# Kernel optimization log

Measured on AMD Instinct MI355X. Metric: run time of the kernel, lower is better.

Reference implementation:

```python
import jax, jax.numpy as jnp
import numpy as np

B, H, S, D = 2, 16, 2048, 64

def setup_inputs() -> dict:
    key = jax.random.key(0)
    kq, kk, kv = jax.random.split(key, 3)
    Q = jax.random.normal(kq, (B, H, S, D), dtype=jnp.float32)
    K = jax.random.normal(kk, (B, H, S, D), dtype=jnp.float32)
    V = jax.random.normal(kv, (B, H, S, D), dtype=jnp.float32)
    # causal mask, broadcastable over batch/head dims (True = keep)
    mask = jnp.tril(jnp.ones((S, S), dtype=jnp.bool_))
    return {"Q": Q, "K": K, "V": V, "mask": mask}

def reference(Q, K, V, mask):
    scale = jax.lax.rsqrt(jnp.float32(Q.shape[-1]))
    # [b, h, q, k] attention logits
    at = jnp.einsum('bhqd,bhkd->bhqk', Q, K) * scale
    at = jnp.where(mask, at, -jnp.inf)
    # manual numerically-stable softmax (matches SoftMax module)
    x_max = jnp.max(at, axis=-1, keepdims=True)
    x_exp = jnp.exp(at - x_max)
    scores = x_exp / jnp.sum(x_exp, axis=-1, keepdims=True)
    return jnp.einsum('bhqk,bhkd->bhqd', scores, V)
```

## Files before the change

### kernel.cpp

```cpp
#include <hip/hip_runtime.h>
#include <math.h>

typedef __attribute__((ext_vector_type(8))) short bf16x8;
typedef __attribute__((ext_vector_type(8))) short s16x8;
typedef __attribute__((ext_vector_type(4))) short s16x4;
typedef __attribute__((ext_vector_type(4))) float f32x4;
typedef __attribute__((ext_vector_type(16))) float f32x16;

namespace {
constexpr int kS   = 2048;
constexpr int kD   = 64;
constexpr int kBH  = 32;
constexpr int kT   = kS / 64;
constexpr int PPAD = 72;
constexpr float kScaleLog2e = 0.125f * 1.44269504088896340736f;
}

__device__ __forceinline__ short f2bf(float f) {
    union { float f; unsigned u; } c; c.f = f;
    unsigned r = c.u + 0x7fffu + ((c.u >> 16) & 1u);
    return (short)(r >> 16);
}

__device__ __forceinline__ s16x8 pack8(const float4& a, const float4& b) {
    s16x8 r;
    r[0] = f2bf(a.x); r[1] = f2bf(a.y); r[2] = f2bf(a.z); r[3] = f2bf(a.w);
    r[4] = f2bf(b.x); r[5] = f2bf(b.y); r[6] = f2bf(b.z); r[7] = f2bf(b.w);
    return r;
}

__device__ __forceinline__ unsigned cvtpk(float lo, float hi_) {
    unsigned r;
    asm("v_cvt_pk_bf16_f32 %0, %1, %2" : "=v"(r) : "v"(lo), "v"(hi_));
    return r;
}
__device__ __forceinline__ void plswap(unsigned& a, unsigned& b) {
    asm("v_permlane32_swap_b32 %0, %1" : "+v"(a), "+v"(b));
}

__global__ __launch_bounds__(256)
void prepack(const float* __restrict__ K, const float* __restrict__ V,
             short* __restrict__ wsK, short* __restrict__ wsVT)
{
    __shared__ float vt[64][65];
    const int tid = threadIdx.x;
    const int kb  = blockIdx.x;
    const int bh  = blockIdx.y;
    const int r   = tid >> 2;
    const int s   = tid & 3;
    const int c0  = s * 16;

    const size_t grow = ((size_t)bh * kS + (size_t)kb * 64 + r) * kD + c0;
    const size_t tbase = ((size_t)bh * kT + kb) * 4096;

    {
        const float4* kr = (const float4*)(K + grow);
        float4 a = kr[0], b = kr[1], c = kr[2], d = kr[3];
        const int kt = r >> 5, ql = r & 31;
        short* out = wsK + tbase + (size_t)((s * 2 + kt) * 64) * 8;
        *(s16x8*)(out + (size_t)ql * 8)        = pack8(a, b);
        *(s16x8*)(out + (size_t)(32 + ql) * 8) = pack8(c, d);
    }
    {
        const float4* vr = (const float4*)(V + grow);
        float4 a = vr[0], b = vr[1], c = vr[2], d = vr[3];
        float t[16] = {a.x,a.y,a.z,a.w, b.x,b.y,b.z,b.w,
                       c.x,c.y,c.z,c.w, d.x,d.y,d.z,d.w};
        #pragma unroll
        for (int jj = 0; jj < 16; ++jj) vt[r][c0 + jj] = t[jj];
    }
    __syncthreads();
    {
        const int d     = tid >> 2;
        const int slice = tid & 3;
        const int k0    = slice * 16;
        const int dt = d >> 5, ql = d & 31;
        s16x8 g0, g1;
        #pragma unroll
        for (int jj = 0; jj < 8; ++jj) g0[jj] = f2bf(vt[k0 + jj][d]);
        #pragma unroll
        for (int jj = 0; jj < 8; ++jj) g1[jj] = f2bf(vt[k0 + 8 + jj][d]);
        short* out = wsVT + tbase + (size_t)((slice * 2 + dt) * 64) * 8;
        *(s16x8*)(out + (size_t)ql * 8)        = g0;
        *(s16x8*)(out + (size_t)(32 + ql) * 8) = g1;
    }
}

__global__ __launch_bounds__(64)
void attn_pair(const float* __restrict__ Q, const short* __restrict__ wsK,
               const short* __restrict__ wsVT, float* __restrict__ O)
{
    const int lane = threadIdx.x & 63;
    const int ql   = lane & 31;
    const int hi   = lane >> 5;

    const int n    = (int)blockIdx.x;
    const int xcd  = n & 7;
    const int rest = n >> 3;
    const int bh   = xcd * 4 + (rest >> 5);
    const int p    = rest & 31;

    const char* Kroot = (const char*)wsK + (size_t)bh * kT * 8192;
    const char* Vroot = (const char*)wsVT + (size_t)bh * kT * 8192;

    f32x16 zero16;
    #pragma unroll
    for (int c = 0; c < 16; ++c) zero16[c] = 0.f;

    auto loadK = [&](int kb, bf16x8 (&kf)[8]) {
        const char* kp = Kroot + (size_t)kb * 8192 + lane * 16;
        #pragma unroll
        for (int i = 0; i < 8; ++i)
            kf[i] = *(const bf16x8*)(kp + i * 1024);
    };

    #pragma unroll 1
    for (int sidx = 0; sidx < 2; ++sidx) {
        const int qs   = sidx == 0 ? 63 - p : p;
        const int T    = (qs >> 1) + 1;
        const int qrow = qs * 32 + ql;

        const float* Qr = Q + ((size_t)bh * kS + qrow) * kD;
        bf16x8 qf[4];
        #pragma unroll
        for (int s = 0; s < 4; ++s) {
            const float4 a = *(const float4*)(Qr + s * 16 + hi * 8);
            const float4 b = *(const float4*)(Qr + s * 16 + hi * 8 + 4);
            bf16x8 f;
            f[0] = f2bf(a.x * kScaleLog2e); f[1] = f2bf(a.y * kScaleLog2e);
            f[2] = f2bf(a.z * kScaleLog2e); f[3] = f2bf(a.w * kScaleLog2e);
            f[4] = f2bf(b.x * kScaleLog2e); f[5] = f2bf(b.y * kScaleLog2e);
            f[6] = f2bf(b.z * kScaleLog2e); f[7] = f2bf(b.w * kScaleLog2e);
            qf[s] = f;
        }

        f32x16 o[2] = {zero16, zero16};
        float l_ = 0.f;

        bf16x8 kA[8], kB[8];
        loadK(0, kA);

        auto tile = [&](bf16x8 (&kcur)[8], bf16x8 (&knxt)[8], int kb) {
            bf16x8 vf[8];
            {
                const char* vp = Vroot + (size_t)kb * 8192 + lane * 16;
                #pragma unroll
                for (int i = 0; i < 8; ++i)
                    vf[i] = *(const bf16x8*)(vp + i * 1024);
            }

            f32x16 sacc[2] = {zero16, zero16};
            #pragma unroll
            for (int kt = 0; kt < 2; ++kt)
                #pragma unroll
                for (int s = 0; s < 4; ++s)
                    sacc[kt] = __builtin_amdgcn_mfma_f32_32x32x16_bf16(
                        kcur[s * 2 + kt], qf[s], sacc[kt], 0, 0, 0);

            if (kb + 1 < T) loadK(kb + 1, knxt);

            if (kb == T - 1) {
                #pragma unroll
                for (int kt = 0; kt < 2; ++kt) {
                    const int kbase = kb * 64 + kt * 32 + 4 * hi;
                    #pragma unroll
                    for (int c = 0; c < 16; ++c) {
                        const int kg = kbase + (c & 3) + 8 * (c >> 2);
                        if (kg > qrow) sacc[kt][c] = -1e30f;
                    }
                }
            }

            float psum = 0.f;
            #pragma unroll
            for (int kt = 0; kt < 2; ++kt)
                #pragma unroll
                for (int c = 0; c < 16; ++c) {
                    const float pe = exp2f(sacc[kt][c]);
                    sacc[kt][c] = pe;
                    psum += pe;
                }
            l_ += psum;

            #pragma unroll
            for (int kt = 0; kt < 2; ++kt) {
                unsigned w8[8];
                #pragma unroll
                for (int i = 0; i < 8; ++i)
                    w8[i] = cvtpk(sacc[kt][2 * i], sacc[kt][2 * i + 1]);
                #pragma unroll
                for (int s = 0; s < 2; ++s) {
                    unsigned A0 = w8[4 * s + 0], B0 = w8[4 * s + 2];
                    unsigned A1 = w8[4 * s + 1], B1 = w8[4 * s + 3];
                    plswap(A0, B0);
                    plswap(A1, B1);
                    union { unsigned u[4]; bf16x8 v; } pk;
                    pk.u[0] = A0; pk.u[1] = A1; pk.u[2] = B0; pk.u[3] = B1;
                    #pragma unroll
                    for (int dt = 0; dt < 2; ++dt)
                        o[dt] = __builtin_amdgcn_mfma_f32_32x32x16_bf16(
                            vf[(kt * 2 + s) * 2 + dt], pk.v, o[dt], 0, 0, 0);
                }
            }
        };

        int kb = 0;
        #pragma unroll 1
        while (true) {
            tile(kA, kB, kb);
            if (++kb == T) break;
            tile(kB, kA, kb);
            if (++kb == T) break;
        }

        const float l   = l_ + __shfl_xor(l_, 32);
        const float inv = 1.0f / l;
        float* Ob = O + ((size_t)bh * kS + qrow) * kD;
        #pragma unroll
        for (int dt = 0; dt < 2; ++dt)
            #pragma unroll
            for (int t = 0; t < 4; ++t) {
                float4 v;
                v.x = o[dt][4 * t + 0] * inv;
                v.y = o[dt][4 * t + 1] * inv;
                v.z = o[dt][4 * t + 2] * inv;
                v.w = o[dt][4 * t + 3] * inv;
                *(float4*)(Ob + dt * 32 + 4 * hi + 8 * t) = v;
            }
    }
}

__global__ __launch_bounds__(256)
void attn_mfma(const float* __restrict__ Q, const float* __restrict__ K,
               const float* __restrict__ V, float* __restrict__ O)
{
    __shared__ short Klds[64 * PPAD];
    __shared__ short VTlds[64 * PPAD];
    __shared__ short Plds[4 * 16 * PPAD];

    const int tid  = threadIdx.x;
    const int lane = tid & 63;
    const int w    = tid >> 6;
    const int lo   = lane & 15;
    const int hi   = lane >> 4;
    const int qt = (int)gridDim.x - 1 - (int)blockIdx.x;
    const int bh = blockIdx.y;
    const size_t hbase = (size_t)bh * kS * kD;

    const float* Qr = Q + hbase + (size_t)(qt * 64 + w * 16 + lo) * kD;
    bf16x8 qfrag[2];
    #pragma unroll
    for (int dc = 0; dc < 2; ++dc) {
        const float4 a = *(const float4*)(Qr + dc * 32 + hi * 8);
        const float4 b = *(const float4*)(Qr + dc * 32 + hi * 8 + 4);
        bf16x8 f;
        f[0] = f2bf(a.x * kScaleLog2e); f[1] = f2bf(a.y * kScaleLog2e);
        f[2] = f2bf(a.z * kScaleLog2e); f[3] = f2bf(a.w * kScaleLog2e);
        f[4] = f2bf(b.x * kScaleLog2e); f[5] = f2bf(b.y * kScaleLog2e);
        f[6] = f2bf(b.z * kScaleLog2e); f[7] = f2bf(b.w * kScaleLog2e);
        qfrag[dc] = f;
    }

    const f32x4 zero4 = {0.f, 0.f, 0.f, 0.f};
    f32x4 o[4] = {zero4, zero4, zero4, zero4};
    float m_[4] = {-1e30f, -1e30f, -1e30f, -1e30f};
    float l_[4] = {0.f, 0.f, 0.f, 0.f};
    const int sr = tid >> 2;
    const int sc = (tid & 3) * 16;
    const float* Kg = K + hbase;
    const float* Vg = V + hbase;
    short* Pw = &Plds[w * 16 * PPAD];

    for (int kb = 0; kb <= qt; ++kb) {
        __syncthreads();
        {
            const float* krow = Kg + (size_t)(kb * 64 + sr) * kD + sc;
            const float* vrow = Vg + (size_t)(kb * 64 + sr) * kD + sc;
            #pragma unroll
            for (int i = 0; i < 4; ++i) {
                const float4 kv = ((const float4*)krow)[i];
                s16x4 ks;
                ks[0] = f2bf(kv.x); ks[1] = f2bf(kv.y);
                ks[2] = f2bf(kv.z); ks[3] = f2bf(kv.w);
                *(s16x4*)&Klds[sr * PPAD + sc + i * 4] = ks;
                const float4 vv = ((const float4*)vrow)[i];
                VTlds[(sc + i * 4 + 0) * PPAD + sr] = f2bf(vv.x);
                VTlds[(sc + i * 4 + 1) * PPAD + sr] = f2bf(vv.y);
                VTlds[(sc + i * 4 + 2) * PPAD + sr] = f2bf(vv.z);
                VTlds[(sc + i * 4 + 3) * PPAD + sr] = f2bf(vv.w);
            }
        }
        __syncthreads();

        f32x4 sacc[4] = {zero4, zero4, zero4, zero4};
        #pragma unroll
        for (int kk = 0; kk < 4; ++kk)
            #pragma unroll
            for (int dc = 0; dc < 2; ++dc) {
                const bf16x8 kf = *(const bf16x8*)(
                    &Klds[(kk * 16 + lo) * PPAD + dc * 32 + hi * 8]);
                sacc[kk] = __builtin_amdgcn_mfma_f32_16x16x32_bf16(
                    qfrag[dc], kf, sacc[kk], 0, 0, 0);
            }
        if (kb == qt) {
            #pragma unroll
            for (int kk = 0; kk < 4; ++kk)
                #pragma unroll
                for (int r = 0; r < 4; ++r)
                    if (kk * 16 + lo > w * 16 + hi * 4 + r) sacc[kk][r] = -1e30f;
        }
        float nm[4], alpha[4];
        #pragma unroll
        for (int r = 0; r < 4; ++r) {
            float v = fmaxf(fmaxf(sacc[0][r], sacc[1][r]),
                            fmaxf(sacc[2][r], sacc[3][r]));
            v = fmaxf(v, __shfl_xor(v, 1));
            v = fmaxf(v, __shfl_xor(v, 2));
            v = fmaxf(v, __shfl_xor(v, 4));
            v = fmaxf(v, __shfl_xor(v, 8));
            nm[r]    = fmaxf(v, m_[r]);
            alpha[r] = exp2f(m_[r] - nm[r]);
        }
        float p[4][4];
        #pragma unroll
        for (int kk = 0; kk < 4; ++kk)
            #pragma unroll
            for (int r = 0; r < 4; ++r)
                p[kk][r] = exp2f(sacc[kk][r] - nm[r]);
        #pragma unroll
        for (int r = 0; r < 4; ++r) {
            float s = (p[0][r] + p[1][r]) + (p[2][r] + p[3][r]);
            s += __shfl_xor(s, 1);
            s += __shfl_xor(s, 2);
            s += __shfl_xor(s, 4);
            s += __shfl_xor(s, 8);
            l_[r] = l_[r] * alpha[r] + s;
            m_[r] = nm[r];
        }
        #pragma unroll
        for (int dcB = 0; dcB < 4; ++dcB)
            #pragma unroll
            for (int r = 0; r < 4; ++r)
                o[dcB][r] *= alpha[r];
        #pragma unroll
        for (int kk = 0; kk < 4; ++kk)
            #pragma unroll
            for (int r = 0; r < 4; ++r)
                Pw[(hi * 4 + r) * PPAD + kk * 16 + lo] = f2bf(p[kk][r]);
        #pragma unroll
        for (int kc = 0; kc < 2; ++kc) {
            const bf16x8 pf = *(const bf16x8*)(&Pw[lo * PPAD + kc * 32 + hi * 8]);
            #pragma unroll
            for (int dcB = 0; dcB < 4; ++dcB) {
                const bf16x8 vf = *(const bf16x8*)(
                    &VTlds[(dcB * 16 + lo) * PPAD + kc * 32 + hi * 8]);
                o[dcB] = __builtin_amdgcn_mfma_f32_16x16x32_bf16(
                    pf, vf, o[dcB], 0, 0, 0);
            }
        }
    }
    float* Ob = O + hbase;
    #pragma unroll
    for (int r = 0; r < 4; ++r) {
        const float inv = 1.0f / l_[r];
        const size_t q = (size_t)(qt * 64 + w * 16 + hi * 4 + r);
        #pragma unroll
        for (int dcB = 0; dcB < 4; ++dcB)
            Ob[q * kD + dcB * 16 + lo] = o[dcB][r] * inv;
    }
}

extern "C" void kernel_launch(void* const* d_in, const int* in_sizes, int n_in,
                              void* d_out, int out_size, void* d_ws, size_t ws_size,
                              hipStream_t stream) {
    const float* Q = (const float*)d_in[0];
    const float* K = (const float*)d_in[1];
    const float* V = (const float*)d_in[2];
    float* out = (float*)d_out;
    (void)in_sizes; (void)n_in; (void)out_size;

    const size_t elemsK   = (size_t)kBH * kS * kD;
    const size_t need_pre = elemsK * 2 * sizeof(short);

    if (ws_size >= need_pre) {
        short* wsK  = (short*)d_ws;
        short* wsVT = wsK + elemsK;
        prepack<<<dim3(kT, kBH), 256, 0, stream>>>(K, V, wsK, wsVT);
        attn_pair<<<dim3(1024), 64, 0, stream>>>(Q, wsK, wsVT, out);
    } else {
        attn_mfma<<<dim3(kT, kBH), 256, 0, stream>>>(Q, K, V, out);
    }
}
```

Measured before the change: 51.57 us.

## Share K tiles across four waves via LDS with async global-to-LDS staging

Replaces the single-wave pair kernel with a 256-thread block of four waves. Each wave handles one 32-row query slab, paired so the causal work per block is balanced. The waves share K tiles double-buffered in LDS, loaded with global_load_lds, instead of each wave reading K into registers on its own. This cuts redundant global K traffic and register pressure. In exchange it adds a block-wide barrier per tile, and waves with shorter causal ranges sit idle until the longest wave finishes.

```diff
diff --git a/kernel.cpp b/kernel.cpp
--- a/kernel.cpp
+++ b/kernel.cpp
@@ -27,6 +27,12 @@
     r[0] = f2bf(a.x); r[1] = f2bf(a.y); r[2] = f2bf(a.z); r[3] = f2bf(a.w);
     r[4] = f2bf(b.x); r[5] = f2bf(b.y); r[6] = f2bf(b.z); r[7] = f2bf(b.w);
     return r;
+}
+
+typedef const __attribute__((address_space(1))) void* gas_t;
+typedef __attribute__((address_space(3))) void* las_t;
+__device__ __forceinline__ void glds16(const void* g, void* l) {
+    __builtin_amdgcn_global_load_lds((gas_t)g, (las_t)l, 16, 0, 0);
 }
 
 __device__ __forceinline__ unsigned cvtpk(float lo, float hi_) {
@@ -86,80 +92,86 @@
     }
 }
 
-__global__ __launch_bounds__(64)
-void attn_pair(const float* __restrict__ Q, const short* __restrict__ wsK,
-               const short* __restrict__ wsVT, float* __restrict__ O)
+__global__ __launch_bounds__(256, 2)
+void attn_v8(const float* __restrict__ Q, const short* __restrict__ wsK,
+             const short* __restrict__ wsVT, float* __restrict__ O)
 {
-    const int lane = threadIdx.x & 63;
+    __shared__ short Kst[2][4096];
+
+    const int tid  = threadIdx.x;
+    const int w    = tid >> 6;
+    const int lane = tid & 63;
     const int ql   = lane & 31;
     const int hi   = lane >> 5;
 
-    const int n    = (int)blockIdx.x;
-    const int xcd  = n & 7;
-    const int rest = n >> 3;
-    const int bh   = xcd * 4 + (rest >> 5);
-    const int p    = rest & 31;
+    const int n   = (int)blockIdx.x;
+    const int xcd = n & 7;
+    const int j   = n >> 3;
+    const int p   = j >> 2;
+    const int bh  = xcd * 4 + (j & 3);
+
+    const int qs   = ((w >> 1) << 5) + ((w & 1) ? (31 - p) : p);
+    const int Tw   = (qs >> 1) + 1;
+    const int Tmax = ((63 - p) >> 1) + 1;
+    const int qrow = qs * 32 + ql;
+
+    const float* Qr = Q + ((size_t)bh * kS + qrow) * kD;
+    bf16x8 qf[4];
+    #pragma unroll
+    for (int s = 0; s < 4; ++s) {
+        const float4 a = *(const float4*)(Qr + s * 16 + hi * 8);
+        const float4 b = *(const float4*)(Qr + s * 16 + hi * 8 + 4);
+        bf16x8 f;
+        f[0] = f2bf(a.x * kScaleLog2e); f[1] = f2bf(a.y * kScaleLog2e);
+        f[2] = f2bf(a.z * kScaleLog2e); f[3] = f2bf(a.w * kScaleLog2e);
+        f[4] = f2bf(b.x * kScaleLog2e); f[5] = f2bf(b.y * kScaleLog2e);
+        f[6] = f2bf(b.z * kScaleLog2e); f[7] = f2bf(b.w * kScaleLog2e);
+        qf[s] = f;
+    }
+
+    f32x16 zero16;
+    #pragma unroll
+    for (int c = 0; c < 16; ++c) zero16[c] = 0.f;
+    f32x16 o[2] = {zero16, zero16};
+    float l_ = 0.f;
 
     const char* Kroot = (const char*)wsK + (size_t)bh * kT * 8192;
     const char* Vroot = (const char*)wsVT + (size_t)bh * kT * 8192;
 
-    f32x16 zero16;
-    #pragma unroll
-    for (int c = 0; c < 16; ++c) zero16[c] = 0.f;
-
-    auto loadK = [&](int kb, bf16x8 (&kf)[8]) {
-        const char* kp = Kroot + (size_t)kb * 8192 + lane * 16;
-        #pragma unroll
-        for (int i = 0; i < 8; ++i)
-            kf[i] = *(const bf16x8*)(kp + i * 1024);
+    auto stageK = [&](int kb, int b) {
+        const char* ks = Kroot + (size_t)kb * 8192 + tid * 16;
+        char* dst = (char*)&Kst[b][0] + tid * 16;
+        glds16(ks,        dst);
+        glds16(ks + 4096, dst + 4096);
     };
 
+    stageK(0, 0);
+    __syncthreads();
+
+    int buf = 0;
     #pragma unroll 1
-    for (int sidx = 0; sidx < 2; ++sidx) {
-        const int qs   = sidx == 0 ? 63 - p : p;
-        const int T    = (qs >> 1) + 1;
-        const int qrow = qs * 32 + ql;
-
-        const float* Qr = Q + ((size_t)bh * kS + qrow) * kD;
-        bf16x8 qf[4];
-        #pragma unroll
-        for (int s = 0; s < 4; ++s) {
-            const float4 a = *(const float4*)(Qr + s * 16 + hi * 8);
-            const float4 b = *(const float4*)(Qr + s * 16 + hi * 8 + 4);
-            bf16x8 f;
-            f[0] = f2bf(a.x * kScaleLog2e); f[1] = f2bf(a.y * kScaleLog2e);
-            f[2] = f2bf(a.z * kScaleLog2e); f[3] = f2bf(a.w * kScaleLog2e);
-            f[4] = f2bf(b.x * kScaleLog2e); f[5] = f2bf(b.y * kScaleLog2e);
-            f[6] = f2bf(b.z * kScaleLog2e); f[7] = f2bf(b.w * kScaleLog2e);
-            qf[s] = f;
-        }
-
-        f32x16 o[2] = {zero16, zero16};
-        float l_ = 0.f;
-
-        bf16x8 kA[8], kB[8];
-        loadK(0, kA);
-
-        auto tile = [&](bf16x8 (&kcur)[8], bf16x8 (&knxt)[8], int kb) {
+    for (int kb = 0; kb < Tmax; ++kb) {
+        if (kb + 1 < Tmax) stageK(kb + 1, buf ^ 1);
+
+        if (kb < Tw) {
+            const char* vp = Vroot + (size_t)kb * 8192 + lane * 16;
             bf16x8 vf[8];
-            {
-                const char* vp = Vroot + (size_t)kb * 8192 + lane * 16;
-                #pragma unroll
-                for (int i = 0; i < 8; ++i)
-                    vf[i] = *(const bf16x8*)(vp + i * 1024);
-            }
-
+            #pragma unroll
+            for (int i = 0; i < 8; ++i)
+                vf[i] = *(const bf16x8*)(vp + i * 1024);
+
+            const char* Kl = (const char*)&Kst[buf][0] + lane * 16;
             f32x16 sacc[2] = {zero16, zero16};
             #pragma unroll
             for (int kt = 0; kt < 2; ++kt)
                 #pragma unroll
-                for (int s = 0; s < 4; ++s)
+                for (int s = 0; s < 4; ++s) {
+                    const bf16x8 kf = *(const bf16x8*)(Kl + (s * 2 + kt) * 1024);
                     sacc[kt] = __builtin_amdgcn_mfma_f32_32x32x16_bf16(
-                        kcur[s * 2 + kt], qf[s], sacc[kt], 0, 0, 0);
-
-            if (kb + 1 < T) loadK(kb + 1, knxt);
-
-            if (kb == T - 1) {
+                        kf, qf[s], sacc[kt], 0, 0, 0);
+                }
+
+            if (kb == Tw - 1) {
                 #pragma unroll
                 for (int kt = 0; kt < 2; ++kt) {
                     const int kbase = kb * 64 + kt * 32 + 4 * hi;
@@ -202,32 +214,25 @@
                             vf[(kt * 2 + s) * 2 + dt], pk.v, o[dt], 0, 0, 0);
                 }
             }
-        };
-
-        int kb = 0;
-        #pragma unroll 1
-        while (true) {
-            tile(kA, kB, kb);
-            if (++kb == T) break;
-            tile(kB, kA, kb);
-            if (++kb == T) break;
-        }
-
-        const float l   = l_ + __shfl_xor(l_, 32);
-        const float inv = 1.0f / l;
-        float* Ob = O + ((size_t)bh * kS + qrow) * kD;
-        #pragma unroll
-        for (int dt = 0; dt < 2; ++dt)
-            #pragma unroll
-            for (int t = 0; t < 4; ++t) {
-                float4 v;
-                v.x = o[dt][4 * t + 0] * inv;
-                v.y = o[dt][4 * t + 1] * inv;
-                v.z = o[dt][4 * t + 2] * inv;
-                v.w = o[dt][4 * t + 3] * inv;
-                *(float4*)(Ob + dt * 32 + 4 * hi + 8 * t) = v;
-            }
-    }
+        }
+        __syncthreads();
+        buf ^= 1;
+    }
+
+    const float l   = l_ + __shfl_xor(l_, 32);
+    const float inv = 1.0f / l;
+    float* Ob = O + ((size_t)bh * kS + qrow) * kD;
+    #pragma unroll
+    for (int dt = 0; dt < 2; ++dt)
+        #pragma unroll
+        for (int t = 0; t < 4; ++t) {
+            float4 v;
+            v.x = o[dt][4 * t + 0] * inv;
+            v.y = o[dt][4 * t + 1] * inv;
+            v.z = o[dt][4 * t + 2] * inv;
+            v.w = o[dt][4 * t + 3] * inv;
+            *(float4*)(Ob + dt * 32 + 4 * hi + 8 * t) = v;
+        }
 }
 
 __global__ __launch_bounds__(256)
@@ -386,7 +391,7 @@
         short* wsK  = (short*)d_ws;
         short* wsVT = wsK + elemsK;
         prepack<<<dim3(kT, kBH), 256, 0, stream>>>(K, V, wsK, wsVT);
-        attn_pair<<<dim3(1024), 64, 0, stream>>>(Q, wsK, wsVT, out);
+        attn_v8<<<dim3(512), 256, 0, stream>>>(Q, wsK, wsVT, out);
     } else {
         attn_mfma<<<dim3(kT, kBH), 256, 0, stream>>>(Q, K, V, out);
     }
```

Measured after the change: 61.02 us. 1.18x slower.

## Split each causal strip pair across two waves with LDS partial-sum merge

Applied to the files above, without the earlier changes.

Each block now runs two waves: one computes the first 17 key tiles of the long query strip, the other computes the short strip and the remaining tiles of the long strip. The second wave's unnormalized partial output and row sum go to shared memory and are added by the first wave before storing. This balances work per wave and doubles the wave count to shorten the per-block serial path. It adds an LDS exchange, a block barrier, and a duplicate Q load for the long strip.

```diff
diff --git a/kernel.cpp b/kernel.cpp
--- a/kernel.cpp
+++ b/kernel.cpp
@@ -86,19 +86,27 @@
     }
 }
 
-__global__ __launch_bounds__(64)
-void attn_pair(const float* __restrict__ Q, const short* __restrict__ wsK,
-               const short* __restrict__ wsVT, float* __restrict__ O)
+__global__ __launch_bounds__(128)
+void attn_v9(const float* __restrict__ Q, const short* __restrict__ wsK,
+             const short* __restrict__ wsVT, float* __restrict__ O)
 {
-    const int lane = threadIdx.x & 63;
+    __shared__ float4 mO[8][64];
+    __shared__ float  mL[64];
+
+    const int tid  = threadIdx.x;
+    const int w    = tid >> 6;
+    const int lane = tid & 63;
     const int ql   = lane & 31;
     const int hi   = lane >> 5;
 
-    const int n    = (int)blockIdx.x;
-    const int xcd  = n & 7;
-    const int rest = n >> 3;
-    const int bh   = xcd * 4 + (rest >> 5);
-    const int p    = rest & 31;
+    const int n   = (int)blockIdx.x;
+    const int xcd = n & 7;
+    const int j   = n >> 3;
+    const int bh  = xcd * 4 + (j >> 5);
+    const int p   = j & 31;
+
+    const int T1 = ((63 - p) >> 1) + 1;
+    const int T2 = (p >> 1) + 1;
 
     const char* Kroot = (const char*)wsK + (size_t)bh * kT * 8192;
     const char* Vroot = (const char*)wsVT + (size_t)bh * kT * 8192;
@@ -107,6 +115,9 @@
     #pragma unroll
     for (int c = 0; c < 16; ++c) zero16[c] = 0.f;
 
+    f32x16 o[2];
+    float  l_;
+
     auto loadK = [&](int kb, bf16x8 (&kf)[8]) {
         const char* kp = Kroot + (size_t)kb * 8192 + lane * 16;
         #pragma unroll
@@ -114,11 +125,10 @@
             kf[i] = *(const bf16x8*)(kp + i * 1024);
     };
 
-    #pragma unroll 1
-    for (int sidx = 0; sidx < 2; ++sidx) {
-        const int qs   = sidx == 0 ? 63 - p : p;
-        const int T    = (qs >> 1) + 1;
-        const int qrow = qs * 32 + ql;
+    auto process = [&](int qs, int kb0, int kb1) {
+        if (kb0 >= kb1) return;
+        const int Tdiag = (qs >> 1) + 1;
+        const int qrow  = qs * 32 + ql;
 
         const float* Qr = Q + ((size_t)bh * kS + qrow) * kD;
         bf16x8 qf[4];
@@ -134,11 +144,8 @@
             qf[s] = f;
         }
 
-        f32x16 o[2] = {zero16, zero16};
-        float l_ = 0.f;
-
         bf16x8 kA[8], kB[8];
-        loadK(0, kA);
+        loadK(kb0, kA);
 
         auto tile = [&](bf16x8 (&kcur)[8], bf16x8 (&knxt)[8], int kb) {
             bf16x8 vf[8];
@@ -157,9 +164,9 @@
                     sacc[kt] = __builtin_amdgcn_mfma_f32_32x32x16_bf16(
                         kcur[s * 2 + kt], qf[s], sacc[kt], 0, 0, 0);
 
-            if (kb + 1 < T) loadK(kb + 1, knxt);
-
-            if (kb == T - 1) {
+            if (kb + 1 < kb1) loadK(kb + 1, knxt);
+
+            if (kb == Tdiag - 1) {
                 #pragma unroll
                 for (int kt = 0; kt < 2; ++kt) {
                     const int kbase = kb * 64 + kt * 32 + 4 * hi;
@@ -204,18 +211,20 @@
             }
         };
 
-        int kb = 0;
+        int kb = kb0;
         #pragma unroll 1
         while (true) {
             tile(kA, kB, kb);
-            if (++kb == T) break;
+            if (++kb == kb1) break;
             tile(kB, kA, kb);
-            if (++kb == T) break;
-        }
-
+            if (++kb == kb1) break;
+        }
+    };
+
+    auto store_strip = [&](int qs) {
         const float l   = l_ + __shfl_xor(l_, 32);
         const float inv = 1.0f / l;
-        float* Ob = O + ((size_t)bh * kS + qrow) * kD;
+        float* Ob = O + ((size_t)bh * kS + qs * 32 + ql) * kD;
         #pragma unroll
         for (int dt = 0; dt < 2; ++dt)
             #pragma unroll
@@ -227,6 +236,46 @@
                 v.w = o[dt][4 * t + 3] * inv;
                 *(float4*)(Ob + dt * 32 + 4 * hi + 8 * t) = v;
             }
+    };
+
+    if (w == 0) {
+        o[0] = zero16; o[1] = zero16; l_ = 0.f;
+        process(63 - p, 0, 17);
+    } else {
+        o[0] = zero16; o[1] = zero16; l_ = 0.f;
+        process(p, 0, T2);
+        store_strip(p);
+        o[0] = zero16; o[1] = zero16; l_ = 0.f;
+        process(63 - p, 17, T1);
+        #pragma unroll
+        for (int dt = 0; dt < 2; ++dt)
+            #pragma unroll
+            for (int t = 0; t < 4; ++t) {
+                float4 v;
+                v.x = o[dt][4 * t + 0];
+                v.y = o[dt][4 * t + 1];
+                v.z = o[dt][4 * t + 2];
+                v.w = o[dt][4 * t + 3];
+                mO[dt * 4 + t][lane] = v;
+            }
+        mL[lane] = l_;
+    }
+
+    __syncthreads();
+
+    if (w == 0) {
+        #pragma unroll
+        for (int dt = 0; dt < 2; ++dt)
+            #pragma unroll
+            for (int t = 0; t < 4; ++t) {
+                const float4 v = mO[dt * 4 + t][lane];
+                o[dt][4 * t + 0] += v.x;
+                o[dt][4 * t + 1] += v.y;
+                o[dt][4 * t + 2] += v.z;
+                o[dt][4 * t + 3] += v.w;
+            }
+        l_ += mL[lane];
+        store_strip(63 - p);
     }
 }
 
@@ -386,7 +435,7 @@
         short* wsK  = (short*)d_ws;
         short* wsVT = wsK + elemsK;
         prepack<<<dim3(kT, kBH), 256, 0, stream>>>(K, V, wsK, wsVT);
-        attn_pair<<<dim3(1024), 64, 0, stream>>>(Q, wsK, wsVT, out);
+        attn_v9<<<dim3(1024), 128, 0, stream>>>(Q, wsK, wsVT, out);
     } else {
         attn_mfma<<<dim3(kT, kBH), 256, 0, stream>>>(Q, K, V, out);
     }
```

New measurement: 51.68 us. Within noise of the previous version (+0.2%).
